# Optimization experiments

Measured on AMD Instinct MI355X. Metric: run time of the kernel, lower is better.

## Reference

```python
import jax, jax.numpy as jnp
import numpy as np

NUM_HEADS = 16
WINDOW = 256  # local_window_size: query i attends keys in [i-WINDOW+1, i]


def setup_inputs() -> dict:
    key = jax.random.key(0)
    ks = jax.random.split(key, 7)
    B, L, D = 2, 2048, 1024
    s = 0.02  # typical init scale for projection weights
    return {
        "hidden_states": jax.random.normal(ks[0], (B, L, D), jnp.float32),
        "Wq": jax.random.normal(ks[1], (D, D), jnp.float32) * s,
        "bq": jnp.zeros((D,), jnp.float32),
        "Wk": jax.random.normal(ks[2], (D, D), jnp.float32) * s,
        "bk": jnp.zeros((D,), jnp.float32),
        "Wv": jax.random.normal(ks[3], (D, D), jnp.float32) * s,
        "bv": jnp.zeros((D,), jnp.float32),
    }


def reference(hidden_states, Wq, bq, Wk, bk, Wv, bv):
    B, L, D = hidden_states.shape
    H = NUM_HEADS
    dh = D // H

    def split_heads(x):  # [B,L,D] -> [B,H,L,dh]
        return x.reshape(B, L, H, dh).transpose(0, 2, 1, 3)

    q = split_heads(hidden_states @ Wq + bq)
    k = split_heads(hidden_states @ Wk + bk)
    v = split_heads(hidden_states @ Wv + bv)

    scores = jnp.einsum("bhqd,bhkd->bhqk", q, k) / jnp.sqrt(jnp.float32(dh))

    # causal sliding-window band: key j visible to query i iff i-WINDOW < j <= i
    i = jnp.arange(L)[:, None]
    j = jnp.arange(L)[None, :]
    band = (j <= i) & (j > i - WINDOW)
    scores = jnp.where(band, scores, -jnp.inf)

    probs = jax.nn.softmax(scores, axis=-1)  # dropout p=0 (eval)
    out = jnp.einsum("bhqk,bhkd->bhqd", probs, v)
    return out.transpose(0, 2, 1, 3).reshape(B, L, D)
```

## Files before the change

kernel.cpp:

```cpp
#include <hip/hip_runtime.h>
#include <hip/hip_bf16.h>
#include <stdint.h>
#include <math.h>

typedef __bf16 bf16;
typedef bf16  bf16x4  __attribute__((ext_vector_type(4)));
typedef bf16  bf16x8  __attribute__((ext_vector_type(8)));
typedef float floatx4 __attribute__((ext_vector_type(4)));

#define MFMA_16x16x32_BF16(a, b, c) \
  __builtin_amdgcn_mfma_f32_16x16x32_bf16((a), (b), (c), 0, 0, 0)

__device__ __forceinline__ int imin(int a, int b) { return a < b ? a : b; }
__device__ __forceinline__ int imax(int a, int b) { return a > b ? a : b; }

__device__ __forceinline__ void load_lds16(const void* g, void* l) {
  __builtin_amdgcn_global_load_lds(
      (const __attribute__((address_space(1))) unsigned int*)g,
      (__attribute__((address_space(3))) unsigned int*)l, 16, 0, 0);
}

#define LSEQ 2048
#define DMODEL 1024
#define NH 16
#define DH 64

__global__ void pack_all(const float4* __restrict__ x, uint16_t* __restrict__ y,
                         const float* __restrict__ Wq, const float* __restrict__ Wk,
                         const float* __restrict__ Wv, uint16_t* __restrict__ Wt) {
  const int bi = blockIdx.x;
  if (bi < 4096) {
    int i = bi * 256 + threadIdx.x;
    float4 f = x[i];
    bf16x4 v;
    v[0] = (bf16)f.x; v[1] = (bf16)f.y; v[2] = (bf16)f.z; v[3] = (bf16)f.w;
    *(bf16x4*)&y[(size_t)i * 4] = v;
    return;
  }
  __shared__ float tile[32][33];
  const int p = bi - 4096;
  const int z = p >> 10;
  const int rem = p & 1023;
  const int k0 = (rem >> 5) * 32, n0 = (rem & 31) * 32;
  const float* W = (z == 0) ? Wq : (z == 1) ? Wk : Wv;
  const int tx = threadIdx.x & 31, ty = threadIdx.x >> 5;
#pragma unroll
  for (int i = 0; i < 4; ++i)
    tile[ty + i * 8][tx] = W[(size_t)(k0 + ty + i * 8) * DMODEL + n0 + tx];
  __syncthreads();
  uint16_t* out = Wt + (size_t)z * DMODEL * DMODEL;
#pragma unroll
  for (int i = 0; i < 4; ++i)
    *(bf16*)&out[(size_t)(n0 + ty + i * 8) * DMODEL + k0 + tx] =
        (bf16)tile[tx][ty + i * 8];
}

__global__ __launch_bounds__(256, 3) void qkv_gemm(
    const uint16_t* __restrict__ A, const uint16_t* __restrict__ Wt,
    const float* __restrict__ bq, const float* __restrict__ bk,
    const float* __restrict__ bv,
    uint16_t* __restrict__ outq, uint16_t* __restrict__ outk,
    uint16_t* __restrict__ outvt) {
  __shared__ __attribute__((aligned(16))) uint16_t lds[17408];
  const int xcd = blockIdx.x & 7;
  const int i = blockIdx.x >> 3;
  const int m0 = (xcd * 4 + (i & 3)) * 128;
  const int rest = i >> 2;
  const int n0 = (rest & 7) * 128;
  const int z = rest >> 3;
  const uint16_t* Bt = Wt + (size_t)z * DMODEL * DMODEL;
  const float* bias = (z == 0) ? bq : (z == 1) ? bk : bv;

  const int t = threadIdx.x;
  const int lane = t & 63;
  const int wave = t >> 6;
  const int wm = (wave >> 1) * 64;
  const int wn = (wave & 1) * 64;
  const int col = lane & 15;
  const int quad = lane >> 4;

  floatx4 acc[4][4] = {};

  auto stage = [&](int kk, int bi) {
    const int k0 = kk * 32;
    uint16_t* base = &lds[bi * 8192];
#pragma unroll
    for (int c = 0; c < 4; ++c) {
      int chunk = t + c * 256;
      int cc = chunk & 511;
      int row = cc >> 2;
      int col16 = (cc & 3) ^ (row & 3);
      const uint16_t* g = (chunk < 512)
          ? A  + (size_t)(m0 + row) * DMODEL + k0 + col16 * 8
          : Bt + (size_t)(n0 + row) * DMODEL + k0 + col16 * 8;
      load_lds16(g, &base[chunk * 8]);
    }
  };

  stage(0, 0);
  for (int kk = 0; kk < 32; ++kk) {
    __syncthreads();
    if (kk < 31) stage(kk + 1, (kk + 1) & 1);
    const uint16_t* base = &lds[(kk & 1) * 8192];

    bf16x8 afrag[4], bfrag[4];
#pragma unroll
    for (int mi = 0; mi < 4; ++mi) {
      int r = wm + mi * 16 + col;
      afrag[mi] = *(const bf16x8*)&base[r * 32 + ((quad ^ (r & 3)) * 8)];
    }
#pragma unroll
    for (int nj = 0; nj < 4; ++nj) {
      int r = wn + nj * 16 + col;
      bfrag[nj] = *(const bf16x8*)&base[4096 + r * 32 + ((quad ^ (r & 3)) * 8)];
    }
#pragma unroll
    for (int mi = 0; mi < 4; ++mi)
#pragma unroll
      for (int nj = 0; nj < 4; ++nj)
        acc[mi][nj] = MFMA_16x16x32_BF16(afrag[mi], bfrag[nj], acc[mi][nj]);
  }

  if (z != 2) {
    const float scale = (z == 0) ? 0.125f : 1.0f;
    uint16_t* outp = (z == 0) ? outq : outk;
#pragma unroll
    for (int nj = 0; nj < 4; ++nj) {
      int gn = n0 + wn + nj * 16 + col;
      float bb = bias[gn];
      int h = gn >> 6, d = gn & 63;
#pragma unroll
      for (int mi = 0; mi < 4; ++mi) {
#pragma unroll
        for (int r = 0; r < 4; ++r) {
          int gm = m0 + wm + mi * 16 + quad * 4 + r;
          int b = gm >> 11, l = gm & 2047;
          *(bf16*)&outp[(((size_t)b * NH + h) * LSEQ + l) * DH + d] =
              (bf16)((acc[mi][nj][r] + bb) * scale);
        }
      }
    }
  } else {
    __syncthreads();
#pragma unroll
    for (int nj = 0; nj < 4; ++nj) {
      int n = wn + nj * 16 + col;
      float bb = bias[n0 + n];
#pragma unroll
      for (int mi = 0; mi < 4; ++mi) {
        int mb = wm + mi * 16 + quad * 4;
        int pp = (mb & ~31) | (((mb >> 2) & 3) << 3) | (((mb >> 4) & 1) << 2);
#pragma unroll
        for (int r = 0; r < 4; ++r)
          *(bf16*)&lds[n * 136 + pp + r] = (bf16)(acc[mi][nj][r] + bb);
      }
    }
    __syncthreads();
    const int n = t >> 1, mh = (t & 1) * 64;
    const int gn = n0 + n, d = gn & 63, h = gn >> 6;
    const int b = m0 >> 11, l0 = (m0 & 2047) + mh;
    uint16_t* dst = &outvt[(((size_t)b * NH + h) * DH + d) * LSEQ + l0];
    const uint16_t* src = &lds[n * 136 + mh];
#pragma unroll
    for (int j = 0; j < 8; ++j)
      *(bf16x8*)&dst[j * 8] = *(const bf16x8*)&src[j * 8];
  }
}

__global__ __launch_bounds__(256, 4) void attn(
    const uint16_t* __restrict__ Q, const uint16_t* __restrict__ K,
    const uint16_t* __restrict__ Vt, float* __restrict__ out) {
  __shared__ __attribute__((aligned(16))) uint16_t kbuf[2][4096];
  __shared__ __attribute__((aligned(16))) uint16_t vbuf[2][4096];

  const int t = threadIdx.x;
  const int lane = t & 63;
  const int w = t >> 6;
  const int xcd = blockIdx.x & 7;
  const int slot = blockIdx.x >> 3;
  const int bh = xcd * 4 + (slot >> 5);
  const int q0 = (slot & 31) * 64;
  const int q0w = q0 + w * 16;
  const int b = bh >> 4, h = bh & 15;
  const uint16_t* Qp = Q + (size_t)bh * LSEQ * DH;
  const uint16_t* Kp = K + (size_t)bh * LSEQ * DH;
  const uint16_t* Vp = Vt + (size_t)bh * DH * LSEQ;
  const int col = lane & 15, quad = lane >> 4;

  bf16x8 qf0 = *(const bf16x8*)&Qp[(size_t)(q0w + col) * DH + quad * 8];
  bf16x8 qf1 = *(const bf16x8*)&Qp[(size_t)(q0w + col) * DH + 32 + quad * 8];

  bf16x8 ones;
#pragma unroll
  for (int u = 0; u < 8; ++u) ones[u] = (bf16)1.0f;

  const int c_start = (q0 < 256) ? ((256 - q0) >> 6) : 0;

  floatx4 o[4] = {};
  floatx4 lac = {0.f, 0.f, 0.f, 0.f};

  auto stage = [&](int c, int bi) {
    const int kc = q0 - 256 + 64 * c;
    int ci = w * 64 + lane;
    {
      int row = ci >> 3, s = ci & 7;
      const uint16_t* g = Kp + (size_t)(kc + row) * DH + ((s ^ (row & 7)) * 8);
      load_lds16(g, &kbuf[bi][w * 512]);
      int row2 = row + 32;
      const uint16_t* g2 = Kp + (size_t)(kc + row2) * DH + ((s ^ (row2 & 7)) * 8);
      load_lds16(g2, &kbuf[bi][2048 + w * 512]);
    }
    {
      int d = ci >> 3, s = ci & 7;
      const uint16_t* g = Vp + (size_t)d * LSEQ + kc + ((s ^ (d & 7)) * 8);
      load_lds16(g, &vbuf[bi][w * 512]);
      int d2 = d + 32;
      const uint16_t* g2 = Vp + (size_t)d2 * LSEQ + kc + ((s ^ (d2 & 7)) * 8);
      load_lds16(g2, &vbuf[bi][2048 + w * 512]);
    }
  };

  stage(c_start, c_start & 1);

  for (int c = c_start; c <= 4; ++c) {
    __syncthreads();
    if (c < 4) stage(c + 1, (c + 1) & 1);

    const int kc = q0 - 256 + 64 * c;
    const int hi = q0w + 15, lo = q0w - 255;
    if (kc <= hi && kc + 64 > lo) {
      const uint16_t* kb_ = kbuf[c & 1];
      const uint16_t* vb_ = vbuf[c & 1];

      floatx4 sT[4] = {{0,0,0,0},{0,0,0,0},{0,0,0,0},{0,0,0,0}};
#pragma unroll
      for (int sub = 0; sub < 4; ++sub) {
        int r_ = sub * 16 + col;
        bf16x8 ka  = *(const bf16x8*)&kb_[r_ * 64 + ((quad ^ (r_ & 7)) * 8)];
        bf16x8 kb2 = *(const bf16x8*)&kb_[r_ * 64 + (((4 + quad) ^ (r_ & 7)) * 8)];
        sT[sub] = MFMA_16x16x32_BF16(ka, qf0, sT[sub]);
        sT[sub] = MFMA_16x16x32_BF16(kb2, qf1, sT[sub]);
      }

      const bool needm = (kc < q0w - 240) | (kc + 63 > q0w);
      const int q = q0w + col;
      bf16x8 pb[2];
#pragma unroll
      for (int sel = 0; sel < 2; ++sel) {
#pragma unroll
        for (int sp = 0; sp < 2; ++sp) {
#pragma unroll
          for (int r = 0; r < 4; ++r) {
            float v = sT[sel * 2 + sp][r];
            if (needm) {
              int key = kc + sel * 32 + sp * 16 + quad * 4 + r;
              v = ((key <= q) & (key > q - 256)) ? v : -INFINITY;
            }
            pb[sel][sp * 4 + r] = (bf16)__expf(v);
          }
        }
      }

#pragma unroll
      for (int nj = 0; nj < 4; ++nj) {
        int d = nj * 16 + col;
        bf16x8 va0 = *(const bf16x8*)&vb_[d * 64 + ((quad ^ (d & 7)) * 8)];
        bf16x8 va1 = *(const bf16x8*)&vb_[d * 64 + (((4 + quad) ^ (d & 7)) * 8)];
        o[nj] = MFMA_16x16x32_BF16(va0, pb[0], o[nj]);
        o[nj] = MFMA_16x16x32_BF16(va1, pb[1], o[nj]);
      }
      lac = MFMA_16x16x32_BF16(ones, pb[0], lac);
      lac = MFMA_16x16x32_BF16(ones, pb[1], lac);
    }
  }

  float rinv = 1.0f / lac[0];
#pragma unroll
  for (int nj = 0; nj < 4; ++nj) {
    float4 v4;
    v4.x = o[nj][0] * rinv; v4.y = o[nj][1] * rinv;
    v4.z = o[nj][2] * rinv; v4.w = o[nj][3] * rinv;
    *(float4*)&out[((size_t)b * LSEQ + q0w + col) * DMODEL + h * DH + nj * 16 + quad * 4] = v4;
  }
}

extern "C" void kernel_launch(void* const* d_in, const int* in_sizes, int n_in,
                              void* d_out, int out_size, void* d_ws, size_t ws_size,
                              hipStream_t stream) {
  const float* hidden = (const float*)d_in[0];
  const float* Wq = (const float*)d_in[1];
  const float* bq = (const float*)d_in[2];
  const float* Wk = (const float*)d_in[3];
  const float* bk = (const float*)d_in[4];
  const float* Wv = (const float*)d_in[5];
  const float* bv = (const float*)d_in[6];
  float* out = (float*)d_out;

  char* ws = (char*)d_ws;
  uint16_t* hb  = (uint16_t*)(ws);
  uint16_t* Wt  = (uint16_t*)(ws + ((size_t)8  << 20));
  uint16_t* qb  = (uint16_t*)(ws + ((size_t)14 << 20));
  uint16_t* kb  = (uint16_t*)(ws + ((size_t)22 << 20));
  uint16_t* vtb = (uint16_t*)(ws + ((size_t)30 << 20));

  pack_all<<<7168, 256, 0, stream>>>((const float4*)hidden, hb, Wq, Wk, Wv, Wt);
  qkv_gemm<<<768, 256, 0, stream>>>(hb, Wt, bq, bk, bv, qb, kb, vtb);
  attn<<<1024, 256, 0, stream>>>(qb, kb, vtb, out);
}
```

Baseline: 132.6 us.

## Use two-wave 64x128 per-wave tiles in QKV GEMM

```diff
diff --git a/kernel.cpp b/kernel.cpp
--- a/kernel.cpp
+++ b/kernel.cpp
@@ -55,13 +55,13 @@
         (bf16)tile[tx][ty + i * 8];
 }
 
-__global__ __launch_bounds__(256, 3) void qkv_gemm(
+__global__ __launch_bounds__(128, 3) void qkv_gemm(
     const uint16_t* __restrict__ A, const uint16_t* __restrict__ Wt,
     const float* __restrict__ bq, const float* __restrict__ bk,
     const float* __restrict__ bv,
     uint16_t* __restrict__ outq, uint16_t* __restrict__ outk,
     uint16_t* __restrict__ outvt) {
-  __shared__ __attribute__((aligned(16))) uint16_t lds[17408];
+  __shared__ __attribute__((aligned(16))) uint16_t lds[16384];
   const int xcd = blockIdx.x & 7;
   const int i = blockIdx.x >> 3;
   const int m0 = (xcd * 4 + (i & 3)) * 128;
@@ -74,19 +74,18 @@
   const int t = threadIdx.x;
   const int lane = t & 63;
   const int wave = t >> 6;
-  const int wm = (wave >> 1) * 64;
-  const int wn = (wave & 1) * 64;
+  const int wm = wave * 64;
   const int col = lane & 15;
   const int quad = lane >> 4;
 
-  floatx4 acc[4][4] = {};
+  floatx4 acc[4][8] = {};
 
   auto stage = [&](int kk, int bi) {
     const int k0 = kk * 32;
     uint16_t* base = &lds[bi * 8192];
 #pragma unroll
-    for (int c = 0; c < 4; ++c) {
-      int chunk = t + c * 256;
+    for (int c = 0; c < 8; ++c) {
+      int chunk = t + c * 128;
       int cc = chunk & 511;
       int row = cc >> 2;
       int col16 = (cc & 3) ^ (row & 3);
@@ -103,30 +102,28 @@
     if (kk < 31) stage(kk + 1, (kk + 1) & 1);
     const uint16_t* base = &lds[(kk & 1) * 8192];
 
-    bf16x8 afrag[4], bfrag[4];
+    bf16x8 afrag[4];
 #pragma unroll
     for (int mi = 0; mi < 4; ++mi) {
       int r = wm + mi * 16 + col;
       afrag[mi] = *(const bf16x8*)&base[r * 32 + ((quad ^ (r & 3)) * 8)];
     }
 #pragma unroll
-    for (int nj = 0; nj < 4; ++nj) {
-      int r = wn + nj * 16 + col;
-      bfrag[nj] = *(const bf16x8*)&base[4096 + r * 32 + ((quad ^ (r & 3)) * 8)];
-    }
-#pragma unroll
-    for (int mi = 0; mi < 4; ++mi)
-#pragma unroll
-      for (int nj = 0; nj < 4; ++nj)
-        acc[mi][nj] = MFMA_16x16x32_BF16(afrag[mi], bfrag[nj], acc[mi][nj]);
+    for (int nj = 0; nj < 8; ++nj) {
+      int r = nj * 16 + col;
+      bf16x8 bfrag = *(const bf16x8*)&base[4096 + r * 32 + ((quad ^ (r & 3)) * 8)];
+#pragma unroll
+      for (int mi = 0; mi < 4; ++mi)
+        acc[mi][nj] = MFMA_16x16x32_BF16(afrag[mi], bfrag, acc[mi][nj]);
+    }
   }
 
   if (z != 2) {
     const float scale = (z == 0) ? 0.125f : 1.0f;
     uint16_t* outp = (z == 0) ? outq : outk;
 #pragma unroll
-    for (int nj = 0; nj < 4; ++nj) {
-      int gn = n0 + wn + nj * 16 + col;
+    for (int nj = 0; nj < 8; ++nj) {
+      int gn = n0 + nj * 16 + col;
       float bb = bias[gn];
       int h = gn >> 6, d = gn & 63;
 #pragma unroll
@@ -143,27 +140,32 @@
   } else {
     __syncthreads();
 #pragma unroll
-    for (int nj = 0; nj < 4; ++nj) {
-      int n = wn + nj * 16 + col;
-      float bb = bias[n0 + n];
-#pragma unroll
-      for (int mi = 0; mi < 4; ++mi) {
-        int mb = wm + mi * 16 + quad * 4;
-        int pp = (mb & ~31) | (((mb >> 2) & 3) << 3) | (((mb >> 4) & 1) << 2);
-#pragma unroll
-        for (int r = 0; r < 4; ++r)
-          *(bf16*)&lds[n * 136 + pp + r] = (bf16)(acc[mi][nj][r] + bb);
-      }
-    }
-    __syncthreads();
-    const int n = t >> 1, mh = (t & 1) * 64;
-    const int gn = n0 + n, d = gn & 63, h = gn >> 6;
-    const int b = m0 >> 11, l0 = (m0 & 2047) + mh;
-    uint16_t* dst = &outvt[(((size_t)b * NH + h) * DH + d) * LSEQ + l0];
-    const uint16_t* src = &lds[n * 136 + mh];
-#pragma unroll
-    for (int j = 0; j < 8; ++j)
-      *(bf16x8*)&dst[j * 8] = *(const bf16x8*)&src[j * 8];
+    for (int p = 0; p < 2; ++p) {
+      if (p) __syncthreads();
+#pragma unroll
+      for (int nj4 = 0; nj4 < 4; ++nj4) {
+        int nj = p * 4 + nj4;
+        int nl = nj4 * 16 + col;
+        float bb = bias[n0 + p * 64 + nl];
+#pragma unroll
+        for (int mi = 0; mi < 4; ++mi) {
+          int mb = wm + mi * 16 + quad * 4;
+          int pp = (mb & ~31) | (((mb >> 2) & 3) << 3) | (((mb >> 4) & 1) << 2);
+#pragma unroll
+          for (int r = 0; r < 4; ++r)
+            *(bf16*)&lds[nl * 136 + pp + r] = (bf16)(acc[mi][nj][r] + bb);
+        }
+      }
+      __syncthreads();
+      const int nl = t >> 1, mh = (t & 1) * 64;
+      const int gn = n0 + p * 64 + nl, d = gn & 63, h = gn >> 6;
+      const int b = m0 >> 11, l0 = (m0 & 2047) + mh;
+      uint16_t* dst = &outvt[(((size_t)b * NH + h) * DH + d) * LSEQ + l0];
+      const uint16_t* src = &lds[nl * 136 + mh];
+#pragma unroll
+      for (int j = 0; j < 8; ++j)
+        *(bf16x8*)&dst[j * 8] = *(const bf16x8*)&src[j * 8];
+    }
   }
 }
 
@@ -304,6 +306,6 @@
   uint16_t* vtb = (uint16_t*)(ws + ((size_t)30 << 20));
 
   pack_all<<<7168, 256, 0, stream>>>((const float4*)hidden, hb, Wq, Wk, Wv, Wt);
-  qkv_gemm<<<768, 256, 0, stream>>>(hb, Wt, bq, bk, bv, qb, kb, vtb);
+  qkv_gemm<<<768, 128, 0, stream>>>(hb, Wt, bq, bk, bv, qb, kb, vtb);
   attn<<<1024, 256, 0, stream>>>(qb, kb, vtb, out);
 }
```

Result: slower. 163.1 us (+23.0%).
